# Performance work log

Hardware: AMD Instinct MI355X
Metric: run time of the kernel (lower is better)

## Reference

```python
import jax, jax.numpy as jnp
import numpy as np

V, E, H, K, B, T = 50000, 256, 256, 9, 128, 512


def lstm_dir(x, lens, Wih, Whh, b):
    # x: [B,T,E] -> h outputs [B,T,H], packed-sequence semantics:
    # state frozen and outputs zeroed for t >= lens[b].
    Bs, Ts, _ = x.shape
    Hh = Whh.shape[1]
    xw = jnp.einsum('bte,ge->btg', x, Wih) + b  # [B,T,4H] precomputed input proj
    valid = jnp.arange(Ts)[None, :] < lens[:, None]  # [B,T]

    def step(carry, inp):
        h, c = carry
        xw_t, v = inp  # [B,4H], [B]
        gates = xw_t + h @ Whh.T
        i, f, g, o = jnp.split(gates, 4, axis=-1)  # torch gate order i,f,g,o
        i = jax.nn.sigmoid(i)
        f = jax.nn.sigmoid(f)
        g = jnp.tanh(g)
        o = jax.nn.sigmoid(o)
        c_new = f * c + i * g
        h_new = o * jnp.tanh(c_new)
        v = v[:, None]
        return (jnp.where(v, h_new, h), jnp.where(v, c_new, c)), h_new * v

    init = (jnp.zeros((Bs, Hh), x.dtype), jnp.zeros((Bs, Hh), x.dtype))
    _, ys = jax.lax.scan(step, init, (jnp.swapaxes(xw, 0, 1), valid.T))
    return jnp.swapaxes(ys, 0, 1)


def reverse_by_len(x, lens):
    # per-row reversal within valid length; padding stays zero
    Ts = x.shape[1]
    t = jnp.arange(Ts)
    idx = jnp.clip(lens[:, None] - 1 - t[None, :], 0, Ts - 1)
    m = t[None, :] < lens[:, None]
    return jnp.take_along_axis(x, idx[:, :, None], axis=1) * m[:, :, None]


def crf_llh(em, tags, lens, start, end, trans):
    # torchcrf forward with reduction='sum': sum_b (gold score - logZ)
    Bs, Ts, Kk = em.shape
    mask = jnp.arange(Ts)[None, :] < lens[:, None]
    em_t = jnp.take_along_axis(em, tags[..., None], axis=-1)[..., 0]  # [B,T]
    score = start[tags[:, 0]] + em_t[:, 0]
    tr = trans[tags[:, :-1], tags[:, 1:]]  # [B,T-1]
    score = score + jnp.sum((tr + em_t[:, 1:]) * mask[:, 1:], axis=1)
    last_tag = jnp.take_along_axis(tags, (lens - 1)[:, None], axis=1)[:, 0]
    score = score + end[last_tag]

    def step(alpha, inp):
        e_t, m_t = inp  # [B,K], [B]
        nxt = jax.nn.logsumexp(alpha[:, :, None] + trans[None, :, :], axis=1) + e_t
        return jnp.where(m_t[:, None], nxt, alpha), None

    alpha0 = start[None, :] + em[:, 0]  # [B,K]
    alpha, _ = jax.lax.scan(step, alpha0,
                            (jnp.swapaxes(em[:, 1:], 0, 1), mask[:, 1:].T))
    logZ = jax.nn.logsumexp(alpha + end[None, :], axis=1)
    return jnp.sum(score - logZ)


def setup_inputs() -> dict:
    key = jax.random.key(0)
    ks = jax.random.split(key, 16)
    sentences = jax.random.randint(ks[0], (B, T), 0, V)
    tags = jax.random.randint(ks[1], (B, T), 0, K)
    length_list = jax.random.randint(ks[2], (B,), 1, T + 1)  # >=1 so mask[:,0] all true
    s = float(1.0 / np.sqrt(H))
    u = lambda k, sh: jax.random.uniform(k, sh, jnp.float32, -s, s)
    emb = jax.random.normal(ks[3], (V, E), jnp.float32) * float(np.sqrt(2.0 / E))
    return dict(
        sentences=sentences, tags=tags, length_list=length_list,
        emb=emb,
        Wih_f=u(ks[4], (4 * H, E)), Whh_f=u(ks[5], (4 * H, H)), b_f=u(ks[6], (4 * H,)),
        Wih_b=u(ks[7], (4 * H, E)), Whh_b=u(ks[8], (4 * H, H)), b_b=u(ks[9], (4 * H,)),
        W_out=u(ks[10], (K, 2 * H)), b_out=u(ks[11], (K,)),
        start=jax.random.uniform(ks[12], (K,), jnp.float32, -0.1, 0.1),
        end=jax.random.uniform(ks[13], (K,), jnp.float32, -0.1, 0.1),
        trans=jax.random.uniform(ks[14], (K, K), jnp.float32, -0.1, 0.1),
    )


def reference(sentences, tags, length_list, emb, Wih_f, Whh_f, b_f,
              Wih_b, Whh_b, b_b, W_out, b_out, start, end, trans):
    x = emb[sentences]  # [B,T,E]
    h_f = lstm_dir(x, length_list, Wih_f, Whh_f, b_f)
    x_rev = reverse_by_len(x, length_list)
    h_b = reverse_by_len(lstm_dir(x_rev, length_list, Wih_b, Whh_b, b_b), length_list)
    hcat = jnp.concatenate([h_f, h_b], axis=-1)  # [B,T,2H]
    # Dropout is identity in eval mode
    em = jnp.einsum('bth,kh->btk', hcat, W_out) + b_out  # [B,T,K]
    return crf_llh(em, tags, length_list, start, end, trans)
```

## Files before the change

### kernel.cpp

```cpp
#include <hip/hip_runtime.h>
#include <hip/hip_bf16.h>

typedef short v8s __attribute__((ext_vector_type(8)));
typedef int   v8i __attribute__((ext_vector_type(8)));
typedef float v4f __attribute__((ext_vector_type(4)));
typedef float v2f __attribute__((ext_vector_type(2)));

#define T_ 512

template<int HI>
__device__ __forceinline__ v2f cvt2(unsigned int wsrc){
  return __builtin_amdgcn_cvt_pk_f32_fp8((int)wsrc, HI);
}
__device__ __forceinline__ v2f rcp2(v2f d){
  return (v2f){__builtin_amdgcn_rcpf(d.x), __builtin_amdgcn_rcpf(d.y)};
}
__device__ __forceinline__ v2f tanh2(v2f x){
  v2f x2 = x*x;
  v2f num = x*(x2 + 27.f);
  v2f den = x2*9.f + 27.f;
  v2f r = num * rcp2(den);
  return (v2f){__builtin_amdgcn_fmed3f(r.x,-1.f,1.f),
               __builtin_amdgcn_fmed3f(r.y,-1.f,1.f)};
}
__device__ __forceinline__ v2f sigm2(v2f x){
  v2f y = x*0.5f;
  v2f y2 = y*y;
  v2f num = y*(y2 + 27.f);
  v2f den = y2*9.f + 27.f;
  v2f r = num * rcp2(den);
  v2f rc = (v2f){__builtin_amdgcn_fmed3f(r.x,-1.f,1.f),
                 __builtin_amdgcn_fmed3f(r.y,-1.f,1.f)};
  return rc*0.5f + 0.5f;
}
__device__ __forceinline__ int pi_col(int p){
  return ((p>>5)<<5) + ((p&1)<<4) + ((p&31)>>1);
}
__device__ __forceinline__ v8i ld32(const void* p){
  uint4 lo = *(const uint4*)p;
  uint4 hi = *(const uint4*)((const char*)p + 16);
  v8i r;
  r[0]=(int)lo.x; r[1]=(int)lo.y; r[2]=(int)lo.z; r[3]=(int)lo.w;
  r[4]=(int)hi.x; r[5]=(int)hi.y; r[6]=(int)hi.z; r[7]=(int)hi.w;
  return r;
}
__device__ __forceinline__ unsigned f2fp4(float x){
  unsigned s = (x < 0.f) ? 8u : 0u;
  float a = fabsf(x);
  unsigned m;
  if      (a < 0.25f) m=0u; else if (a < 0.75f) m=1u;
  else if (a < 1.25f) m=2u; else if (a < 1.75f) m=3u;
  else if (a < 2.5f ) m=4u; else if (a < 3.5f ) m=5u;
  else if (a < 5.f  ) m=6u; else m=7u;
  return s|m;
}
__device__ __forceinline__ unsigned pk8(float a, float b, float c, float d){
  int w = __builtin_amdgcn_cvt_pk_fp8_f32(a, b, 0, 0);
  w     = __builtin_amdgcn_cvt_pk_fp8_f32(c, d, w, 1);
  return (unsigned)w;
}
__device__ __forceinline__ unsigned enc4(v2f h){
  v2f t = h*4.f;
  unsigned b = 0;
  #pragma unroll
  for (int s=0;s<2;++s){
    float v = s ? t.y : t.x;
    float ax = __builtin_amdgcn_fmed3f(fabsf(v), 0.f, 4.f);
    float gl = fmaf(ax, 2.f, 12582912.f);
    float gh = ax + 12582912.f;
    unsigned ql = __builtin_bit_cast(unsigned, gl) & 7u;
    unsigned qh = (__builtin_bit_cast(unsigned, gh) & 7u) + 2u;
    unsigned c  = (ax > 1.75f) ? qh : ql;
    unsigned sg = (__builtin_bit_cast(unsigned, v) >> 28) & 8u;
    b |= (c | sg) << (4*s);
  }
  return b;
}

__global__ __launch_bounds__(256) void prep_wih8_k(
    const float* __restrict__ Wa, const float* __restrict__ Wb,
    unsigned char* __restrict__ out)
{
  int idx = blockIdx.x*256 + threadIdx.x;
  int lane = idx & 63;
  int t2 = idx >> 6;
  int ntile = t2 & 127;
  int kt = t2 >> 7;
  int n = ntile*16 + (lane&15);
  const float* W = (n < 1024) ? (Wa + (size_t)n*256) : (Wb + (size_t)(n-1024)*256);
  int k0 = kt*128 + (lane>>4)*32;
  unsigned words[8];
  #pragma unroll
  for (int e=0;e<8;++e)
    words[e] = pk8(W[k0+e*4], W[k0+e*4+1], W[k0+e*4+2], W[k0+e*4+3]);
  unsigned char* d = out + (size_t)idx*32;
  *(uint4*)(d)      = make_uint4(words[0], words[1], words[2], words[3]);
  *(uint4*)(d + 16) = make_uint4(words[4], words[5], words[6], words[7]);
}

__global__ __launch_bounds__(256) void prep_whh4_k(
    const float* __restrict__ Wf, const float* __restrict__ Wb,
    unsigned char* __restrict__ out)
{
  int idx = blockIdx.x*256 + threadIdx.x;
  int lane = idx & 63;
  int t2 = idx >> 6;
  int ntile = t2 & 63;
  int kt = (t2>>6) & 1;
  int dir = t2 >> 7;
  const float* W = dir ? Wb : Wf;
  int n = ntile*16 + (lane&15);
  int kbase = kt*128 + (lane>>4)*32;
  const float* row = W + (size_t)n*256;
  unsigned words[4];
  #pragma unroll
  for (int d4=0;d4<4;++d4){
    unsigned acc = 0;
    #pragma unroll
    for (int j=0;j<8;++j){
      float v = row[pi_col(kbase + d4*8 + j)] * 64.f;
      acc |= f2fp4(v) << (4*j);
    }
    words[d4] = acc;
  }
  *(uint4*)(out + (size_t)idx*16) = make_uint4(words[0], words[1], words[2], words[3]);
}

__global__ __launch_bounds__(256) void xw_gemm_k(
    const int* __restrict__ sent, const float* __restrict__ emb,
    const unsigned char* __restrict__ wihg, const int* __restrict__ lens,
    const float* __restrict__ bfv, const float* __restrict__ bbv,
    unsigned char* __restrict__ xw)
{
  int mt = blockIdx.x;
  if (((mt&3)<<7) >= lens[mt>>2]) return;
  __shared__ unsigned char A[128][272];
  int tid = threadIdx.x;
  {
    int row = tid>>1, half = tid&1;
    int tok = sent[mt*128 + row];
    const float4* s = (const float4*)(emb + (size_t)tok*256 + half*128);
    unsigned char* drow = &A[row][half*128];
    #pragma unroll
    for (int c4=0; c4<8; ++c4){
      unsigned w0[4];
      #pragma unroll
      for (int u=0; u<4; ++u){
        float4 v = s[c4*4+u];
        w0[u] = pk8(v.x, v.y, v.z, v.w);
      }
      *(uint4*)(drow + c4*16) = make_uint4(w0[0], w0[1], w0[2], w0[3]);
    }
  }
  __syncthreads();
  int w = tid>>6, lane = tid&63, lr = lane&15, lq = lane>>4;
  #pragma unroll 1
  for (int i4=0; i4<4; ++i4){
    int dnv = w*4 + i4;
    int dn = dnv>>3, v = dnv&7;
    const float* bb = dn ? bbv : bfv;
    float bias[8];
    #pragma unroll
    for (int e=0;e<8;++e){
      int q = e>>1, s = e&1;
      bias[e] = bb[q*256 + v*32 + s*16 + lr];
    }
    #pragma unroll 1
    for (int mh=0; mh<2; ++mh){
      v4f acc[8][4];
      #pragma unroll
      for (int e=0;e<8;++e)
        #pragma unroll
        for (int mm=0;mm<4;++mm) acc[e][mm] = (v4f){0.f,0.f,0.f,0.f};
      #pragma unroll
      for (int kt=0;kt<2;++kt){
        v8i a0 = ld32(&A[mh*64 +  0 + lr][kt*128 + lq*32]);
        v8i a1 = ld32(&A[mh*64 + 16 + lr][kt*128 + lq*32]);
        v8i a2 = ld32(&A[mh*64 + 32 + lr][kt*128 + lq*32]);
        v8i a3 = ld32(&A[mh*64 + 48 + lr][kt*128 + lq*32]);
        #pragma unroll
        for (int e=0;e<8;++e){
          int q = e>>1, s = e&1;
          int ntile = dn*64 + q*16 + v*2 + s;
          v8i bfr = ld32(wihg + ((size_t)(kt*128 + ntile)*64 + lane)*32);
          acc[e][0] = __builtin_amdgcn_mfma_scale_f32_16x16x128_f8f6f4(
                        a0, bfr, acc[e][0], 0,0, 0,0x7f7f7f7f, 0,0x7f7f7f7f);
          acc[e][1] = __builtin_amdgcn_mfma_scale_f32_16x16x128_f8f6f4(
                        a1, bfr, acc[e][1], 0,0, 0,0x7f7f7f7f, 0,0x7f7f7f7f);
          acc[e][2] = __builtin_amdgcn_mfma_scale_f32_16x16x128_f8f6f4(
                        a2, bfr, acc[e][2], 0,0, 0,0x7f7f7f7f, 0,0x7f7f7f7f);
          acc[e][3] = __builtin_amdgcn_mfma_scale_f32_16x16x128_f8f6f4(
                        a3, bfr, acc[e][3], 0,0, 0,0x7f7f7f7f, 0,0x7f7f7f7f);
        }
      }
      #pragma unroll
      for (int mm=0;mm<4;++mm){
        #pragma unroll
        for (int j=0;j<4;++j){
          int row = mt*128 + mh*64 + mm*16 + lq*4 + j;
          unsigned lo = pk8(acc[0][mm][j]+bias[0], acc[1][mm][j]+bias[1],
                            acc[2][mm][j]+bias[2], acc[3][mm][j]+bias[3]);
          unsigned hi = pk8(acc[4][mm][j]+bias[4], acc[5][mm][j]+bias[5],
                            acc[6][mm][j]+bias[6], acc[7][mm][j]+bias[7]);
          *(uint2*)(xw + ((size_t)dn*65536 + row)*1024 + v*128 + lr*8)
              = make_uint2(lo, hi);
        }
      }
    }
  }
}

__global__ __launch_bounds__(512,1) void lstm_k(
    const unsigned char* __restrict__ xw,
    const unsigned char* __restrict__ whh4,
    const int* __restrict__ lens,
    unsigned char* __restrict__ hout)
{
  int bid = blockIdx.x, dir = bid>>5, grp = bid&31;
  int tid = threadIdx.x, w = tid>>6, lane = tid&63, lr = lane&15, lq = lane>>4;
  __shared__ unsigned char hbuf[2][16][136];
  __shared__ int tmax_s;
  for (int i=tid*4; i<2*16*136; i+=512*4) *(unsigned int*)(&((unsigned char*)hbuf)[i]) = 0u;
  if (tid==0){
    int mx=0;
    for (int i=0;i<4;++i){ int l = lens[grp*4+i]; mx = l>mx? l:mx; }
    tmax_s = mx;
  }
  v8i wreg[16];
  const unsigned char* wb = whh4 + (size_t)dir*131072;
  #pragma unroll
  for (int kt=0;kt<2;++kt){
    #pragma unroll
    for (int nt=0;nt<8;++nt){
      int ntile = (nt>>1)*16 + w*2 + (nt&1);
      uint4 t = *(const uint4*)(wb + ((size_t)(kt*64 + ntile)*64 + lane)*16);
      v8i r;
      r[0]=(int)t.x; r[1]=(int)t.y; r[2]=(int)t.z; r[3]=(int)t.w;
      r[4]=0; r[5]=0; r[6]=0; r[7]=0;
      wreg[kt*8+nt] = r;
    }
  }
  #pragma unroll
  for (int i=0;i<16;++i) asm volatile("" : "+v"(wreg[i]));
  int seq = grp*4 + lq;
  int ln = lens[seq];
  v2f cc = (v2f){0.f, 0.f};
  const size_t dbase = (size_t)dir*65536;
  const unsigned char* xbase = xw + (dbase + (size_t)seq*T_)*1024 + w*128 + lr*8;
  unsigned char* hbase = hout + (dbase + (size_t)seq*T_)*256 + w*32 + lr*2;
  unsigned char* lw0 = &hbuf[1][lq*4][w*16 + lr];
  unsigned char* lw1 = &hbuf[0][lq*4][w*16 + lr];
  const unsigned char* lr0 = &hbuf[0][lr][lq*16];
  const unsigned char* lr1 = &hbuf[1][lr][lq*16];
  __syncthreads();
  int tmax = tmax_s;
  uint2 xv = *(const uint2*)(xbase + (size_t)(dir ? (ln-1) : 0)*1024);

  #define STEP_BODY(TE_EXPR, POS_EXPR)                                         \
    int cur = t&1;                                                             \
    int tn = (t+1<tmax)? t+1 : t;                                              \
    int te = (TE_EXPR);                                                        \
    uint2 xn = *(const uint2*)(xbase + ((size_t)te<<10));                      \
    const unsigned char* lrd = cur? lr1 : lr0;                                 \
    v2f xi = cvt2<0>(xv.x), xf = cvt2<1>(xv.x);                                \
    v2f xg = cvt2<0>(xv.y), xo = cvt2<1>(xv.y);                                \
    v4f acc[8];                                                                \
    _Pragma("unroll")                                                          \
    for (int nt=0;nt<8;++nt) asm("" : "=v"(acc[nt]));                          \
    acc[0][0] = xi.x; acc[1][0] = xi.y;                                        \
    acc[2][0] = xf.x; acc[3][0] = xf.y;                                        \
    acc[4][0] = xg.x; acc[5][0] = xg.y;                                        \
    acc[6][0] = xo.x; acc[7][0] = xo.y;                                        \
    _Pragma("unroll")                                                          \
    for (int kt=0;kt<2;++kt){                                                  \
      uint4 hh = *(const uint4*)(lrd + kt*64);                                 \
      v8i a;                                                                   \
      a[0]=(int)hh.x; a[1]=(int)hh.y; a[2]=(int)hh.z; a[3]=(int)hh.w;          \
      a[4]=0; a[5]=0; a[6]=0; a[7]=0;                                          \
      _Pragma("unroll")                                                        \
      for (int nt=0;nt<8;++nt)                                                 \
        acc[nt] = __builtin_amdgcn_mfma_scale_f32_16x16x128_f8f6f4(            \
                    a, wreg[kt*8+nt], acc[nt], 4, 4,                           \
                    0, 0x7D7D7D7D, 0, 0x79797979);                             \
    }                                                                          \
    int pos = (POS_EXPR);                                                      \
    v2f gi = (v2f){acc[0][0], acc[1][0]};                                      \
    v2f gf = (v2f){acc[2][0], acc[3][0]};                                      \
    v2f gg = (v2f){acc[4][0], acc[5][0]};                                      \
    v2f go = (v2f){acc[6][0], acc[7][0]};                                      \
    v2f iv = sigm2(gi), fv = sigm2(gf), gv = tanh2(gg), ov = sigm2(go);        \
    v2f cn = fv*cc + iv*gv;                                                    \
    v2f hn = ov*tanh2(cn);                                                     \
    cc = cn;                                                                   \
    *(cur? lw1 : lw0) = (unsigned char)enc4(hn);                               \
    int hp = __builtin_amdgcn_cvt_pk_fp8_f32(hn.x, hn.y, 0, 0);                \
    *(unsigned short*)(hbase + ((size_t)pos<<8)) = (unsigned short)(hp&0xffff);\
    xv = xn;                                                                   \
    asm volatile("s_waitcnt lgkmcnt(0)" ::: "memory");                         \
    __builtin_amdgcn_s_barrier();                                              \
    __builtin_amdgcn_sched_barrier(0);

  if (dir == 0){
    for (int t=0; t<tmax; ++t){
      STEP_BODY(tn, t)
    }
  } else {
    for (int t=0; t<tmax; ++t){
      STEP_BODY((tn<ln)? (ln-1-tn) : tn, (t<ln)? (ln-1-t) : t)
    }
  }
  #undef STEP_BODY
}

__global__ __launch_bounds__(256) void em_k(
    const unsigned char* __restrict__ hout,
    const float* __restrict__ Wout, const float* __restrict__ bout,
    const int* __restrict__ lens,
    float* __restrict__ em)
{
  __shared__ float Ws[9*512];
  for (int i=threadIdx.x;i<9*512;i+=256){
    int k = i>>9, p = i&511;
    int d = p>>8, pp = p&255;
    Ws[i] = Wout[k*512 + d*256 + pi_col(pp)];
  }
  __syncthreads();
  int wv = blockIdx.x*4 + (threadIdx.x>>6);
  int lane = threadIdx.x & 63;
  int g = lane>>4, r = lane&15;
  int m = wv*4 + g;
  const unsigned char* hf = hout + (size_t)m*256 + r*16;
  const unsigned char* hb = hout + ((size_t)65536 + m)*256 + r*16;
  uint4 vf = *(const uint4*)hf;
  uint4 vb = *(const uint4*)hb;
  float xf[16], xb[16];
  {
    v2f d0=cvt2<0>(vf.x), d1=cvt2<1>(vf.x), d2=cvt2<0>(vf.y), d3=cvt2<1>(vf.y);
    v2f d4=cvt2<0>(vf.z), d5=cvt2<1>(vf.z), d6=cvt2<0>(vf.w), d7=cvt2<1>(vf.w);
    xf[0]=d0.x; xf[1]=d0.y; xf[2]=d1.x; xf[3]=d1.y;
    xf[4]=d2.x; xf[5]=d2.y; xf[6]=d3.x; xf[7]=d3.y;
    xf[8]=d4.x; xf[9]=d4.y; xf[10]=d5.x; xf[11]=d5.y;
    xf[12]=d6.x; xf[13]=d6.y; xf[14]=d7.x; xf[15]=d7.y;
  }
  {
    v2f d0=cvt2<0>(vb.x), d1=cvt2<1>(vb.x), d2=cvt2<0>(vb.y), d3=cvt2<1>(vb.y);
    v2f d4=cvt2<0>(vb.z), d5=cvt2<1>(vb.z), d6=cvt2<0>(vb.w), d7=cvt2<1>(vb.w);
    xb[0]=d0.x; xb[1]=d0.y; xb[2]=d1.x; xb[3]=d1.y;
    xb[4]=d2.x; xb[5]=d2.y; xb[6]=d3.x; xb[7]=d3.y;
    xb[8]=d4.x; xb[9]=d4.y; xb[10]=d5.x; xb[11]=d5.y;
    xb[12]=d6.x; xb[13]=d6.y; xb[14]=d7.x; xb[15]=d7.y;
  }
  float a[9];
  #pragma unroll
  for (int k=0;k<9;++k){
    float s = 0.f;
    #pragma unroll
    for (int e=0;e<16;++e)
      s += xf[e]*Ws[k*512 + r*16 + e] + xb[e]*Ws[k*512 + 256 + r*16 + e];
    a[k]=s;
  }
  #pragma unroll
  for (int k=0;k<9;++k){
    #pragma unroll
    for (int off=8; off; off>>=1) a[k] += __shfl_xor(a[k], off, 64);
  }
  int b = m>>9, t = m&511;
  if (r==0 && t < lens[b]){
    float* d = em + (size_t)m*9;
    #pragma unroll
    for (int k=0;k<9;++k) d[k] = a[k] + bout[k];
  }
}

__global__ __launch_bounds__(256) void crf_k(
    const float* __restrict__ em, const int* __restrict__ tags,
    const int* __restrict__ lens, const float* __restrict__ startv,
    const float* __restrict__ endv, const float* __restrict__ trans,
    float* __restrict__ out)
{
  int wid = blockIdx.x*4 + (threadIdx.x>>6);
  int lane = threadIdx.x & 63;
  const float* e = em + (size_t)wid*T_*9;
  const int* tg = tags + (size_t)wid*T_;
  int L = lens[wid];
  float p = 0.f;
  for (int t = 1+lane; t < L; t += 64)
    p += trans[tg[t-1]*9 + tg[t]] + e[(size_t)t*9 + tg[t]];
  if (lane==0) p += startv[tg[0]] + e[tg[0]] + endv[tg[L-1]];
  #pragma unroll
  for (int off=32; off; off>>=1) p += __shfl_xor(p, off, 64);
  float tcol[9];
  #pragma unroll
  for (int i=0;i<9;++i) tcol[i] = (lane<9) ? trans[i*9 + lane] : 0.f;
  float alpha = (lane<9) ? (startv[lane] + e[lane]) : -1e30f;
  for (int t=1; t<L; ++t){
    float vs[9]; float mx = -1e30f;
    #pragma unroll
    for (int i=0;i<9;++i){
      float ai = __shfl(alpha, i, 64);
      vs[i] = ai + tcol[i];
      mx = fmaxf(mx, vs[i]);
    }
    float s = 0.f;
    #pragma unroll
    for (int i=0;i<9;++i) s += __expf(vs[i]-mx);
    float na = mx + __logf(s) + ((lane<9)? e[(size_t)t*9+lane] : 0.f);
    alpha = (lane<9) ? na : -1e30f;
  }
  float v = (lane<9) ? (alpha + endv[lane]) : -1e30f;
  float mx = v;
  #pragma unroll
  for (int off=32; off; off>>=1) mx = fmaxf(mx, __shfl_xor(mx, off, 64));
  float s = __expf(v-mx);
  #pragma unroll
  for (int off=32; off; off>>=1) s += __shfl_xor(s, off, 64);
  float logZ = mx + __logf(s);
  if (lane==0) atomicAdd(out, p - logZ);
}

extern "C" void kernel_launch(void* const* d_in, const int* in_sizes, int n_in,
                              void* d_out, int out_size, void* d_ws, size_t ws_size,
                              hipStream_t stream)
{
  const int*   sent  = (const int*)d_in[0];
  const int*   tags  = (const int*)d_in[1];
  const int*   lens  = (const int*)d_in[2];
  const float* emb   = (const float*)d_in[3];
  const float* Wih_f = (const float*)d_in[4];
  const float* Whh_f = (const float*)d_in[5];
  const float* b_f   = (const float*)d_in[6];
  const float* Wih_b = (const float*)d_in[7];
  const float* Whh_b = (const float*)d_in[8];
  const float* b_b   = (const float*)d_in[9];
  const float* Wout  = (const float*)d_in[10];
  const float* bout  = (const float*)d_in[11];
  const float* startv= (const float*)d_in[12];
  const float* endv  = (const float*)d_in[13];
  const float* trans = (const float*)d_in[14];
  char* ws = (char*)d_ws;
  unsigned char* wihg8 = (unsigned char*)(ws);
  unsigned char* whh4  = (unsigned char*)(ws + (size_t)524288);
  unsigned char* xw    = (unsigned char*)(ws + (size_t)1048576);
  unsigned char* hout  = (unsigned char*)(ws + (size_t)135266304);
  float* em            = (float*)(ws + (size_t)168820736);
  float* outp = (float*)d_out;

  (void)hipMemsetAsync(outp, 0, sizeof(float), stream);
  prep_wih8_k<<<64, 256, 0, stream>>>(Wih_f, Wih_b, wihg8);
  prep_whh4_k<<<64, 256, 0, stream>>>(Whh_f, Whh_b, whh4);
  xw_gemm_k<<<512, 256, 0, stream>>>(sent, emb, wihg8, lens, b_f, b_b, xw);
  lstm_k<<<64, 512, 0, stream>>>(xw, whh4, lens, hout);
  em_k<<<4096, 256, 0, stream>>>(hout, Wout, bout, lens, em);
  crf_k<<<32, 256, 0, stream>>>(em, tags, lens, startv, endv, trans, outp);
}
```

Measured before the change: 700.7 us.

## Merge weight prep kernels, simplify sigmoid, and make LSTM wave index uniform

Combines the two weight-packing kernels into one launch with a block-index split, removing one kernel launch and its dependency gap. Rewrites the rational sigmoid approximation to fold the 0.5 scaling into its constants, which drops a multiply and an FMA per gate. In the LSTM kernel, the wave index is marked wave-uniform with readfirstlane and the lane offset is hoisted, so address arithmetic can move to scalar registers. Numerics of the sigmoid stay algebraically equivalent apart from rounding.

```diff
diff --git a/kernel.cpp b/kernel.cpp
--- a/kernel.cpp
+++ b/kernel.cpp
@@ -24,14 +24,13 @@
                __builtin_amdgcn_fmed3f(r.y,-1.f,1.f)};
 }
 __device__ __forceinline__ v2f sigm2(v2f x){
-  v2f y = x*0.5f;
-  v2f y2 = y*y;
-  v2f num = y*(y2 + 27.f);
-  v2f den = y2*9.f + 27.f;
+  v2f x2 = x*x;
+  v2f num = x*(x2 + 108.f);
+  v2f den = x2*36.f + 432.f;
   v2f r = num * rcp2(den);
-  v2f rc = (v2f){__builtin_amdgcn_fmed3f(r.x,-1.f,1.f),
-                 __builtin_amdgcn_fmed3f(r.y,-1.f,1.f)};
-  return rc*0.5f + 0.5f;
+  v2f rc = (v2f){__builtin_amdgcn_fmed3f(r.x,-0.5f,0.5f),
+                 __builtin_amdgcn_fmed3f(r.y,-0.5f,0.5f)};
+  return rc + 0.5f;
 }
 __device__ __forceinline__ int pi_col(int p){
   return ((p>>5)<<5) + ((p&1)<<4) + ((p&31)>>1);
@@ -77,53 +76,52 @@
   return b;
 }
 
-__global__ __launch_bounds__(256) void prep_wih8_k(
-    const float* __restrict__ Wa, const float* __restrict__ Wb,
-    unsigned char* __restrict__ out)
-{
-  int idx = blockIdx.x*256 + threadIdx.x;
-  int lane = idx & 63;
-  int t2 = idx >> 6;
-  int ntile = t2 & 127;
-  int kt = t2 >> 7;
-  int n = ntile*16 + (lane&15);
-  const float* W = (n < 1024) ? (Wa + (size_t)n*256) : (Wb + (size_t)(n-1024)*256);
-  int k0 = kt*128 + (lane>>4)*32;
-  unsigned words[8];
-  #pragma unroll
-  for (int e=0;e<8;++e)
-    words[e] = pk8(W[k0+e*4], W[k0+e*4+1], W[k0+e*4+2], W[k0+e*4+3]);
-  unsigned char* d = out + (size_t)idx*32;
-  *(uint4*)(d)      = make_uint4(words[0], words[1], words[2], words[3]);
-  *(uint4*)(d + 16) = make_uint4(words[4], words[5], words[6], words[7]);
-}
-
-__global__ __launch_bounds__(256) void prep_whh4_k(
-    const float* __restrict__ Wf, const float* __restrict__ Wb,
-    unsigned char* __restrict__ out)
-{
-  int idx = blockIdx.x*256 + threadIdx.x;
-  int lane = idx & 63;
-  int t2 = idx >> 6;
-  int ntile = t2 & 63;
-  int kt = (t2>>6) & 1;
-  int dir = t2 >> 7;
-  const float* W = dir ? Wb : Wf;
-  int n = ntile*16 + (lane&15);
-  int kbase = kt*128 + (lane>>4)*32;
-  const float* row = W + (size_t)n*256;
-  unsigned words[4];
-  #pragma unroll
-  for (int d4=0;d4<4;++d4){
-    unsigned acc = 0;
-    #pragma unroll
-    for (int j=0;j<8;++j){
-      float v = row[pi_col(kbase + d4*8 + j)] * 64.f;
-      acc |= f2fp4(v) << (4*j);
-    }
-    words[d4] = acc;
-  }
-  *(uint4*)(out + (size_t)idx*16) = make_uint4(words[0], words[1], words[2], words[3]);
+__global__ __launch_bounds__(256) void prep_k(
+    const float* __restrict__ WihA, const float* __restrict__ WihB,
+    const float* __restrict__ WhhF, const float* __restrict__ WhhB,
+    unsigned char* __restrict__ wih_out, unsigned char* __restrict__ whh_out)
+{
+  int blk = blockIdx.x;
+  if (blk < 64){
+    int idx = blk*256 + threadIdx.x;
+    int lane = idx & 63;
+    int t2 = idx >> 6;
+    int ntile = t2 & 127;
+    int kt = t2 >> 7;
+    int n = ntile*16 + (lane&15);
+    const float* W = (n < 1024) ? (WihA + (size_t)n*256) : (WihB + (size_t)(n-1024)*256);
+    int k0 = kt*128 + (lane>>4)*32;
+    unsigned words[8];
+    #pragma unroll
+    for (int e=0;e<8;++e)
+      words[e] = pk8(W[k0+e*4], W[k0+e*4+1], W[k0+e*4+2], W[k0+e*4+3]);
+    unsigned char* d = wih_out + (size_t)idx*32;
+    *(uint4*)(d)      = make_uint4(words[0], words[1], words[2], words[3]);
+    *(uint4*)(d + 16) = make_uint4(words[4], words[5], words[6], words[7]);
+  } else {
+    int idx = (blk-64)*256 + threadIdx.x;
+    int lane = idx & 63;
+    int t2 = idx >> 6;
+    int ntile = t2 & 63;
+    int kt = (t2>>6) & 1;
+    int dir = t2 >> 7;
+    const float* W = dir ? WhhB : WhhF;
+    int n = ntile*16 + (lane&15);
+    int kbase = kt*128 + (lane>>4)*32;
+    const float* row = W + (size_t)n*256;
+    unsigned words[4];
+    #pragma unroll
+    for (int d4=0;d4<4;++d4){
+      unsigned acc = 0;
+      #pragma unroll
+      for (int j=0;j<8;++j){
+        float v = row[pi_col(kbase + d4*8 + j)] * 64.f;
+        acc |= f2fp4(v) << (4*j);
+      }
+      words[d4] = acc;
+    }
+    *(uint4*)(whh_out + (size_t)idx*16) = make_uint4(words[0], words[1], words[2], words[3]);
+  }
 }
 
 __global__ __launch_bounds__(256) void xw_gemm_k(
@@ -218,6 +216,7 @@
 {
   int bid = blockIdx.x, dir = bid>>5, grp = bid&31;
   int tid = threadIdx.x, w = tid>>6, lane = tid&63, lr = lane&15, lq = lane>>4;
+  int wu = __builtin_amdgcn_readfirstlane(w);
   __shared__ unsigned char hbuf[2][16][136];
   __shared__ int tmax_s;
   for (int i=tid*4; i<2*16*136; i+=512*4) *(unsigned int*)(&((unsigned char*)hbuf)[i]) = 0u;
@@ -227,13 +226,13 @@
     tmax_s = mx;
   }
   v8i wreg[16];
-  const unsigned char* wb = whh4 + (size_t)dir*131072;
+  const unsigned char* wb = whh4 + (size_t)dir*131072 + (size_t)lane*16;
   #pragma unroll
   for (int kt=0;kt<2;++kt){
     #pragma unroll
     for (int nt=0;nt<8;++nt){
-      int ntile = (nt>>1)*16 + w*2 + (nt&1);
-      uint4 t = *(const uint4*)(wb + ((size_t)(kt*64 + ntile)*64 + lane)*16);
+      int ntile = (nt>>1)*16 + wu*2 + (nt&1);
+      uint4 t = *(const uint4*)(wb + (size_t)(kt*64 + ntile)*1024);
       v8i r;
       r[0]=(int)t.x; r[1]=(int)t.y; r[2]=(int)t.z; r[3]=(int)t.w;
       r[4]=0; r[5]=0; r[6]=0; r[7]=0;
@@ -246,10 +245,10 @@
   int ln = lens[seq];
   v2f cc = (v2f){0.f, 0.f};
   const size_t dbase = (size_t)dir*65536;
-  const unsigned char* xbase = xw + (dbase + (size_t)seq*T_)*1024 + w*128 + lr*8;
-  unsigned char* hbase = hout + (dbase + (size_t)seq*T_)*256 + w*32 + lr*2;
-  unsigned char* lw0 = &hbuf[1][lq*4][w*16 + lr];
-  unsigned char* lw1 = &hbuf[0][lq*4][w*16 + lr];
+  const unsigned char* xbase = xw + (dbase + (size_t)seq*T_)*1024 + wu*128 + lr*8;
+  unsigned char* hbase = hout + (dbase + (size_t)seq*T_)*256 + wu*32 + lr*2;
+  unsigned char* lw0 = &hbuf[1][lq*4][wu*16 + lr];
+  unsigned char* lw1 = &hbuf[0][lq*4][wu*16 + lr];
   const unsigned char* lr0 = &hbuf[0][lr][lq*16];
   const unsigned char* lr1 = &hbuf[1][lr][lq*16];
   __syncthreads();
@@ -446,8 +445,7 @@
   float* outp = (float*)d_out;
 
   (void)hipMemsetAsync(outp, 0, sizeof(float), stream);
-  prep_wih8_k<<<64, 256, 0, stream>>>(Wih_f, Wih_b, wihg8);
-  prep_whh4_k<<<64, 256, 0, stream>>>(Whh_f, Whh_b, whh4);
+  prep_k<<<128, 256, 0, stream>>>(Wih_f, Wih_b, Whh_f, Whh_b, wihg8, whh4);
   xw_gemm_k<<<512, 256, 0, stream>>>(sent, emb, wihg8, lens, b_f, b_b, xw);
   lstm_k<<<64, 512, 0, stream>>>(xw, whh4, lens, hout);
   em_k<<<4096, 256, 0, stream>>>(hout, Wout, bout, lens, em);
```

After: 721.6 us. 1.03x slower.
